# Optimization experiments

Measured on AMD Instinct MI355X. Metric: run time of the kernel, lower is better.

## Reference

```python
import jax, jax.numpy as jnp
import numpy as np

BIG = 1.0e9   # sentinel for masked distances / masked max
K_NBR = 64    # max_num_neighbors in radius()


def _fps(pos, n_sample):
    """Farthest point sampling on a single cloud pos [N, D] -> int32 [n_sample]."""
    n = pos.shape[0]

    def body(i, st):
        d, idxs = st
        last = pos[idxs[i - 1]]                              # [D]
        d = jnp.minimum(d, jnp.sum((pos - last) ** 2, axis=-1))
        return d, idxs.at[i].set(jnp.argmax(d).astype(jnp.int32))

    d0 = jnp.full((n,), BIG, pos.dtype)
    idxs0 = jnp.zeros((n_sample,), jnp.int32)
    _, idxs = jax.lax.fori_loop(1, n_sample, body, (d0, idxs0))
    return idxs


def _mlp2(h, w1, b1, w2, b2):
    # PyG MLP([a,b,c]) in eval mode (dropout off, batch-norm at default running
    # stats == identity): Linear -> ReLU -> Linear (plain last layer).
    return jax.nn.relu(h @ w1 + b1) @ w2 + b2


_gather = jax.vmap(lambda a, i: a[i])  # per-cloud fancy gather


def _sa(x, pos, ratio, r, w1, b1, w2, b2):
    """SAModule: FPS -> radius neighbors (<=K) -> PointConv (gather, MLP on
    [x_j, pos_j - pos_i], max-aggregate). Dense batched: x [B,N,C], pos [B,N,D]."""
    B, N, D = pos.shape
    M = int(round(N * ratio))
    idx = jax.vmap(lambda p: _fps(p, M))(pos)                 # [B, M]
    pos_q = _gather(pos, idx)                                 # [B, M, D]
    # pairwise squared distances query -> all points  [B, M, N]
    d2 = jnp.sum((pos_q[:, :, None, :] - pos[:, None, :, :]) ** 2, axis=-1)
    neg = jnp.where(d2 <= r * r, -d2, -BIG)
    vals, nbr = jax.lax.top_k(neg, K_NBR)                     # [B, M, K]
    valid = vals > -0.5 * BIG                                 # in-radius mask
    x_j = _gather(x, nbr)                                     # [B, M, K, C]
    rel = _gather(pos, nbr) - pos_q[:, :, None, :]            # [B, M, K, D]
    h = _mlp2(jnp.concatenate([x_j, rel], axis=-1), w1, b1, w2, b2)
    h = jnp.where(valid[..., None], h, -BIG)
    return jnp.max(h, axis=2), pos_q                          # max aggregation


def setup_inputs() -> dict:
    key = jax.random.key(0)
    ks = jax.random.split(key, 12)
    B, N, D, F = 8, 4096, 2, 5

    def lin(k, fi, fo):
        return (jax.random.normal(k, (fi, fo), jnp.float32) / np.sqrt(fi)).astype(jnp.float32)

    return {
        "x": jax.random.normal(ks[0], (B, N, F), jnp.float32),
        "pos": jax.random.uniform(ks[1], (B, N, D), jnp.float32),
        # sa1: MLP([5+2, 32, 64])
        "w1a": lin(ks[2], 7, 32),   "b1a": jnp.zeros((32,), jnp.float32),
        "w1b": lin(ks[3], 32, 64),  "b1b": jnp.zeros((64,), jnp.float32),
        # sa2: MLP([64+2, 64, 128])
        "w2a": lin(ks[4], 66, 64),  "b2a": jnp.zeros((64,), jnp.float32),
        "w2b": lin(ks[5], 64, 128), "b2b": jnp.zeros((128,), jnp.float32),
        # sa3 (global): MLP([128+2, 128, 256])
        "w3a": lin(ks[6], 130, 128), "b3a": jnp.zeros((128,), jnp.float32),
        "w3b": lin(ks[7], 128, 256), "b3b": jnp.zeros((256,), jnp.float32),
        # head: MLP([256, 256, 1024], norm=None)
        "w4a": lin(ks[8], 256, 256),  "b4a": jnp.zeros((256,), jnp.float32),
        "w4b": lin(ks[9], 256, 1024), "b4b": jnp.zeros((1024,), jnp.float32),
    }


def reference(x, pos, w1a, b1a, w1b, b1b, w2a, b2a, w2b, b2b,
              w3a, b3a, w3b, b3b, w4a, b4a, w4b, b4b):
    h1, p1 = _sa(x, pos, 0.5, 0.2, w1a, b1a, w1b, b1b)       # [B, N/2, 64]
    h2, p2 = _sa(h1, p1, 0.25, 0.4, w2a, b2a, w2b, b2b)      # [B, N/8, 128]
    g = _mlp2(jnp.concatenate([h2, p2], axis=-1), w3a, b3a, w3b, b3b)
    g = jnp.max(g, axis=1)                                    # global max pool [B, 256]
    return _mlp2(g, w4a, b4a, w4b, b4b)                       # [B, 1024]
```

## Files before the change

kernel.cpp:

```cpp
#include <hip/hip_runtime.h>


#define DPP_UMAX(u, ctrl)                                                      \
  do {                                                                         \
    unsigned _o = (unsigned)__builtin_amdgcn_update_dpp(0, (int)(u), (ctrl),   \
                                                        0xf, 0xf, true);       \
    (u) = ((u) > _o) ? (u) : _o;                                               \
  } while (0)

__device__ __forceinline__ uint4 kmax4(uint4 a, uint4 b) {
  unsigned long long ka = ((unsigned long long)a.y << 32) | a.x;
  unsigned long long kb = ((unsigned long long)b.y << 32) | b.x;
  bool c = kb > ka;
  uint4 r;
  r.x = c ? b.x : a.x; r.y = c ? b.y : a.y;
  r.z = c ? b.z : a.z; r.w = c ? b.w : a.w;
  return r;
}

template<int PPT, int T>
__device__ __forceinline__ void fps_stage(
    float (&xr)[PPT], float (&yr)[PPT], int Msel, int t,
    const float* srcx, const float* srcy,
    float* wlx, float* wly,
    uint4* slots ) {
  constexpr int NW = T / 64;
  constexpr int HP = PPT / 2;
  float lx = srcx[0], ly = srcy[0];
  if (t == 0) { wlx[0] = lx; wly[0] = ly; }
  float d[PPT];
#pragma unroll
  for (int k = 0; k < PPT; ++k) d[k] = 1e9f;

  for (int i = 1; i < Msel; ++i) {
#pragma unroll
    for (int k = 0; k < PPT; ++k) {
      float dx = xr[k] - lx, dy = yr[k] - ly;
      float dd = __fadd_rn(__fmul_rn(dx, dx), __fmul_rn(dy, dy));
      d[k] = fminf(d[k], dd);
    }
    float bvA = d[0]; int bkA = 0;
    float bvB = d[HP]; int bkB = HP;
#pragma unroll
    for (int k = 1; k < HP; ++k) {
      if (d[k] > bvA)      { bvA = d[k];      bkA = k; }
      if (d[HP + k] > bvB) { bvB = d[HP + k]; bkB = HP + k; }
    }
    float bv = bvA; int bk = bkA;
    if (bvB > bvA) { bv = bvB; bk = bkB; }
    const int cand = t * PPT + bk;
    const float cx = srcx[cand], cy = srcy[cand];
    const unsigned mybits = __float_as_uint(bv);
    unsigned u = mybits;
    DPP_UMAX(u, 0x111);
    DPP_UMAX(u, 0x112);
    DPP_UMAX(u, 0x114);
    DPP_UMAX(u, 0x118);
    DPP_UMAX(u, 0x142);
    DPP_UMAX(u, 0x143);
    const unsigned wvb = (unsigned)__builtin_amdgcn_readlane((int)u, 63);
    const unsigned long long tmask = __ballot(mybits == wvb);
    const int fl = (int)__builtin_ctzll(tmask);
    const int widx = __builtin_amdgcn_readlane(cand, fl);
    const unsigned wcx =
        (unsigned)__builtin_amdgcn_readlane((int)__float_as_uint(cx), fl);
    const unsigned wcy =
        (unsigned)__builtin_amdgcn_readlane((int)__float_as_uint(cy), fl);
    const int par = i & 1;
    if ((t & 63) == 0)
      slots[par * NW + (t >> 6)] = make_uint4(~(unsigned)widx, wvb, wcx, wcy);
    __syncthreads();
    const uint4* sl = &slots[par * NW];
    uint4 arr[NW];
#pragma unroll
    for (int j = 0; j < NW; ++j) arr[j] = sl[j];
#pragma unroll
    for (int s = NW / 2; s >= 1; s >>= 1)
#pragma unroll
      for (int j = 0; j < s; ++j) arr[j] = kmax4(arr[j], arr[j + s]);
    lx = __uint_as_float(arr[0].z);
    ly = __uint_as_float(arr[0].w);
    if (t == 0) { wlx[i] = lx; wly[i] = ly; }
  }
}

template<int N, int M1, int M2, int T>
__global__ __launch_bounds__(T, 1) void fps_fused_kernel(
    const float* __restrict__ pos,
    float* __restrict__ posq1,
    float* __restrict__ posq2) {
  constexpr int PPT  = N / T;
  constexpr int PPT2 = M1 / T;
  constexpr int NW   = T / 64;
  __shared__ float sx[N], sy[N];
  __shared__ float wlx[M1], wly[M1];
  __shared__ float wl2x[M2], wl2y[M2];
  __shared__ uint4 slots[2 * NW];
  const int b = blockIdx.x, t = threadIdx.x;
  float xr[PPT], yr[PPT];
  const float4* p4 = (const float4*)(pos + (size_t)b * N * 2 + (size_t)t * PPT * 2);
#pragma unroll
  for (int q = 0; q < PPT / 2; ++q) {
    float4 v = p4[q];
    xr[2 * q + 0] = v.x; yr[2 * q + 0] = v.y;
    xr[2 * q + 1] = v.z; yr[2 * q + 1] = v.w;
  }
#pragma unroll
  for (int k = 0; k < PPT; ++k) {
    int pt = t * PPT + k;
    sx[pt] = xr[k]; sy[pt] = yr[k];
  }
  __syncthreads();
  fps_stage<PPT, T>(xr, yr, M1, t, sx, sy, wlx, wly, slots);
  __syncthreads();
  for (int j = t; j < M1; j += T)
    ((float2*)posq1)[(size_t)b * M1 + j] = make_float2(wlx[j], wly[j]);
  float x2[PPT2], y2[PPT2];
#pragma unroll
  for (int k = 0; k < PPT2; ++k) { x2[k] = wlx[t * PPT2 + k]; y2[k] = wly[t * PPT2 + k]; }
  __syncthreads();
  fps_stage<PPT2, T>(x2, y2, M2, t, wlx, wly, wl2x, wl2y, slots);
  __syncthreads();
  for (int j = t; j < M2; j += T)
    ((float2*)posq2)[(size_t)b * M2 + j] = make_float2(wl2x[j], wl2y[j]);
}

template<int CPL>
__global__ __launch_bounds__(256) void nbr_kernel(
    const float* __restrict__ pts,
    const float* __restrict__ posq,
    int* __restrict__ nbr,
    int M, int NPTS, int total_q, float R2) {
  const int wid = blockIdx.x * 4 + (threadIdx.x >> 6);
  if (wid >= total_q) return;
  const int lane = threadIdx.x & 63;
  const int b = wid / M;
  const float qx = posq[(size_t)wid * 2 + 0], qy = posq[(size_t)wid * 2 + 1];
  const float* p = pts + (size_t)b * NPTS * 2;
  unsigned bits[CPL];
  int cnt = 0;
#pragma unroll
  for (int k = 0; k < CPL; ++k) {
    int pt = lane + (k << 6);
    float dx = p[pt * 2 + 0] - qx, dy = p[pt * 2 + 1] - qy;
    float dd = __fadd_rn(__fmul_rn(dx, dx), __fmul_rn(dy, dy));
    bool inr = (dd <= R2);
    bits[k] = inr ? __float_as_uint(dd) : 0xFFFFFFFFu;
    cnt += __popcll(__ballot(inr));
  }
  const unsigned long long below = (1ULL << lane) - 1ULL;
  if (cnt <= 64) {
    int base = 0;
#pragma unroll
    for (int k = 0; k < CPL; ++k) {
      bool s = (bits[k] != 0xFFFFFFFFu);
      unsigned long long m = __ballot(s);
      if (s) nbr[(size_t)wid * 64 + base + __popcll(m & below)] = lane + (k << 6);
      base += __popcll(m);
    }
    for (int j = base + lane; j < 64; j += 64) nbr[(size_t)wid * 64 + j] = -1;
  } else {
    unsigned lo = 0, hi = __float_as_uint(R2);
    while (lo < hi) {
      unsigned mid = lo + ((hi - lo) >> 1);
      int c = 0;
#pragma unroll
      for (int k = 0; k < CPL; ++k) c += __popcll(__ballot(bits[k] <= mid));
      if (c >= 64) hi = mid; else lo = mid + 1;
    }
    int cless = 0;
#pragma unroll
    for (int k = 0; k < CPL; ++k) cless += __popcll(__ballot(bits[k] < lo));
    const int need = 64 - cless;
    int base = 0, tiecnt = 0;
#pragma unroll
    for (int k = 0; k < CPL; ++k) {
      bool tie = (bits[k] == lo);
      unsigned long long tm = __ballot(tie);
      bool s = (bits[k] < lo) || (tie && (tiecnt + __popcll(tm & below)) < need);
      tiecnt += __popcll(tm);
      unsigned long long m = __ballot(s);
      if (s) nbr[(size_t)wid * 64 + base + __popcll(m & below)] = lane + (k << 6);
      base += __popcll(m);
    }
  }
}

template<int CIN, int H, int COUT, int QPB, int NPTS, int HS, int W1P>
__global__ __launch_bounds__(64 * QPB) void conv_kernel(
    const float* __restrict__ x,
    const float* __restrict__ pts,
    const float* __restrict__ posq,
    const int* __restrict__ nbr,
    const float* __restrict__ W1, const float* __restrict__ b1,
    const float* __restrict__ W2, const float* __restrict__ b2,
    float* __restrict__ out,
    int M) {
  constexpr int CI2 = CIN + 2;
  __shared__ float sW1t[H * W1P];
  __shared__ float sB1[H];
  __shared__ float sHH[QPB * 64 * HS];
  const int tid = threadIdx.x;
  for (int j = tid; j < CI2 * H; j += 64 * QPB) {
    int c = j / H, h = j - c * H;
    sW1t[h * W1P + c] = W1[j];
  }
  for (int j = tid; j < H; j += 64 * QPB) sB1[j] = b1[j];
  __syncthreads();
  const int wv = tid >> 6, lane = tid & 63;
  const int wid = blockIdx.x * QPB + wv;
  const int b = wid / M;
  const int idx = nbr[(size_t)wid * 64 + lane];
  const unsigned long long vm = __ballot(idx >= 0);
  const int ii = (idx < 0) ? 0 : idx;
  float in[CI2];
  {
    const float* xp = x + ((size_t)b * NPTS + ii) * CIN;
#pragma unroll
    for (int c = 0; c < CIN; ++c) in[c] = xp[c];
    float qx = posq[(size_t)wid * 2 + 0], qy = posq[(size_t)wid * 2 + 1];
    const float* pp = pts + ((size_t)b * NPTS + ii) * 2;
    in[CIN] = pp[0] - qx;
    in[CIN + 1] = pp[1] - qy;
  }
  float* hbase = &sHH[wv * 64 * HS];
#pragma unroll
  for (int h = 0; h < H; h += 4) {
    float vv[4];
#pragma unroll
    for (int j = 0; j < 4; ++j) {
      float a = sB1[h + j];
#pragma unroll
      for (int c = 0; c < CI2; ++c) a = fmaf(in[c], sW1t[(h + j) * W1P + c], a);
      vv[j] = fmaxf(a, 0.0f);
    }
    *(float4*)&hbase[lane * HS + h] = make_float4(vv[0], vv[1], vv[2], vv[3]);
  }
#pragma unroll
  for (int half = 0; half < COUT / 64; ++half) {
    const int o = half * 64 + lane;
    float w2r[H];
#pragma unroll
    for (int h = 0; h < H; ++h) w2r[h] = W2[h * COUT + o];
    const float b2o = b2[o];
    float m = -1e30f;
    for (int n = 0; n < 64; ++n) {
      const float4* hp = (const float4*)&hbase[n * HS];
      float a = b2o;
#pragma unroll
      for (int j = 0; j < H / 4; ++j) {
        float4 hv = hp[j];
        a = fmaf(hv.x, w2r[4 * j + 0], a);
        a = fmaf(hv.y, w2r[4 * j + 1], a);
        a = fmaf(hv.z, w2r[4 * j + 2], a);
        a = fmaf(hv.w, w2r[4 * j + 3], a);
      }
      a = ((vm >> n) & 1ULL) ? a : -1e9f;
      m = fmaxf(m, a);
    }
    out[(size_t)wid * COUT + o] = m;
  }
}

__global__ __launch_bounds__(256) void u_kernel(
    const float* __restrict__ h2,
    const float* __restrict__ posq2,
    const float* __restrict__ W3a, const float* __restrict__ b3a,
    float* __restrict__ u) {
  const int p = blockIdx.x * 2 + (threadIdx.x >> 7);
  const int h = threadIdx.x & 127;
  const float* hp = h2 + (size_t)p * 128;
  float a = b3a[h];
  for (int c = 0; c < 128; ++c) a = fmaf(hp[c], W3a[c * 128 + h], a);
  a = fmaf(posq2[(size_t)p * 2 + 0], W3a[128 * 128 + h], a);
  a = fmaf(posq2[(size_t)p * 2 + 1], W3a[129 * 128 + h], a);
  u[(size_t)p * 128 + h] = fmaxf(a, 0.0f);
}

__global__ __launch_bounds__(256) void g_kernel(
    const float* __restrict__ u,
    const float* __restrict__ W3b, const float* __restrict__ b3b,
    float* __restrict__ part) {
  __shared__ float su[64 * 128];
  const int bb = blockIdx.x;
  const float* up = u + (size_t)bb * 64 * 128;
  for (int j = threadIdx.x; j < 64 * 128; j += 256) su[j] = up[j];
  __syncthreads();
  const int o = threadIdx.x;
  float w[128];
#pragma unroll
  for (int h = 0; h < 128; ++h) w[h] = W3b[h * 256 + o];
  float m = -1e30f;
  for (int p = 0; p < 64; ++p) {
    float a = b3b[o];
    const float4* sp = (const float4*)&su[p * 128];
#pragma unroll
    for (int j = 0; j < 32; ++j) {
      float4 v = sp[j];
      a = fmaf(v.x, w[4 * j + 0], a);
      a = fmaf(v.y, w[4 * j + 1], a);
      a = fmaf(v.z, w[4 * j + 2], a);
      a = fmaf(v.w, w[4 * j + 3], a);
    }
    m = fmaxf(m, a);
  }
  part[(size_t)bb * 256 + o] = m;
}

__global__ __launch_bounds__(256) void head_kernel(
    const float* __restrict__ part,
    const float* __restrict__ W4a, const float* __restrict__ b4a,
    const float* __restrict__ W4b, const float* __restrict__ b4b,
    float* __restrict__ out) {
  __shared__ float g[256], h4[256];
  const int b = blockIdx.x, t = threadIdx.x;
  float m = part[(size_t)(b * 8 + 0) * 256 + t];
  for (int c = 1; c < 8; ++c) m = fmaxf(m, part[(size_t)(b * 8 + c) * 256 + t]);
  g[t] = m;
  __syncthreads();
  float a = b4a[t];
  for (int c = 0; c < 256; ++c) a = fmaf(g[c], W4a[c * 256 + t], a);
  h4[t] = fmaxf(a, 0.0f);
  __syncthreads();
  for (int jj = 0; jj < 4; ++jj) {
    int o = t + jj * 256;
    float a2 = b4b[o];
    for (int c = 0; c < 256; ++c) a2 = fmaf(h4[c], W4b[c * 1024 + o], a2);
    out[(size_t)b * 1024 + o] = a2;
  }
}

extern "C" void kernel_launch(void* const* d_in, const int* in_sizes, int n_in,
                              void* d_out, int out_size, void* d_ws, size_t ws_size,
                              hipStream_t stream) {
  (void)in_sizes; (void)n_in; (void)out_size; (void)ws_size;
  const float* x   = (const float*)d_in[0];
  const float* pos = (const float*)d_in[1];
  const float* w1a = (const float*)d_in[2];  const float* b1a = (const float*)d_in[3];
  const float* w1b = (const float*)d_in[4];  const float* b1b = (const float*)d_in[5];
  const float* w2a = (const float*)d_in[6];  const float* b2a = (const float*)d_in[7];
  const float* w2b = (const float*)d_in[8];  const float* b2b = (const float*)d_in[9];
  const float* w3a = (const float*)d_in[10]; const float* b3a = (const float*)d_in[11];
  const float* w3b = (const float*)d_in[12]; const float* b3b = (const float*)d_in[13];
  const float* w4a = (const float*)d_in[14]; const float* b4a = (const float*)d_in[15];
  const float* w4b = (const float*)d_in[16]; const float* b4b = (const float*)d_in[17];
  float* outp = (float*)d_out;

  char* ws = (char*)d_ws;
  size_t off = 0;
  float* posq1 = (float*)(ws + off); off += (size_t)8 * 2048 * 2 * 4;
  float* posq2 = (float*)(ws + off); off += (size_t)8 * 512 * 2 * 4;
  int*   nbr1  = (int*)  (ws + off); off += (size_t)16384 * 64 * 4;
  int*   nbr2  = (int*)  (ws + off); off += (size_t)4096 * 64 * 4;
  float* h1    = (float*)(ws + off); off += (size_t)16384 * 64 * 4;
  float* h2    = (float*)(ws + off); off += (size_t)4096 * 128 * 4;
  float* u3    = (float*)(ws + off); off += (size_t)4096 * 128 * 4;
  float* part  = (float*)(ws + off); off += (size_t)64 * 256 * 4;

  fps_fused_kernel<4096, 2048, 512, 512><<<dim3(8), dim3(512), 0, stream>>>(
      pos, posq1, posq2);
  nbr_kernel<64><<<dim3(4096), dim3(256), 0, stream>>>(pos, posq1, nbr1,
                                                       2048, 4096, 16384, 0.04f);
  conv_kernel<5, 32, 64, 4, 4096, 36, 8><<<dim3(4096), dim3(256), 0, stream>>>(
      x, pos, posq1, nbr1, w1a, b1a, w1b, b1b, h1, 2048);
  nbr_kernel<32><<<dim3(1024), dim3(256), 0, stream>>>(posq1, posq2, nbr2,
                                                       512, 2048, 4096, 0.16f);
  conv_kernel<64, 64, 128, 2, 2048, 68, 68><<<dim3(2048), dim3(128), 0, stream>>>(
      h1, posq1, posq2, nbr2, w2a, b2a, w2b, b2b, h2, 512);
  u_kernel<<<dim3(2048), dim3(256), 0, stream>>>(h2, posq2, w3a, b3a, u3);
  g_kernel<<<dim3(64), dim3(256), 0, stream>>>(u3, w3b, b3b, part);
  head_kernel<<<dim3(8), dim3(256), 0, stream>>>(part, w4a, b4a, w4b, b4b, outp);
}
```

Before: 2.387 ms.

## Carry FPS candidate coordinates in registers and halve the FPS block size

```diff
diff --git a/kernel.cpp b/kernel.cpp
--- a/kernel.cpp
+++ b/kernel.cpp
@@ -21,13 +21,12 @@
 template<int PPT, int T>
 __device__ __forceinline__ void fps_stage(
     float (&xr)[PPT], float (&yr)[PPT], int Msel, int t,
-    const float* srcx, const float* srcy,
+    float lx, float ly,
     float* wlx, float* wly,
     uint4* slots ) {
   constexpr int NW = T / 64;
   constexpr int HP = PPT / 2;
-  float lx = srcx[0], ly = srcy[0];
-  if (t == 0) { wlx[0] = lx; wly[0] = ly; }
+  const int wvid = t >> 6;
   float d[PPT];
 #pragma unroll
   for (int k = 0; k < PPT; ++k) d[k] = 1e9f;
@@ -39,17 +38,15 @@
       float dd = __fadd_rn(__fmul_rn(dx, dx), __fmul_rn(dy, dy));
       d[k] = fminf(d[k], dd);
     }
-    float bvA = d[0]; int bkA = 0;
-    float bvB = d[HP]; int bkB = HP;
+    float bvA = d[0],  bxA = xr[0],  byA = yr[0];
+    float bvB = d[HP], bxB = xr[HP], byB = yr[HP];
 #pragma unroll
     for (int k = 1; k < HP; ++k) {
-      if (d[k] > bvA)      { bvA = d[k];      bkA = k; }
-      if (d[HP + k] > bvB) { bvB = d[HP + k]; bkB = HP + k; }
-    }
-    float bv = bvA; int bk = bkA;
-    if (bvB > bvA) { bv = bvB; bk = bkB; }
-    const int cand = t * PPT + bk;
-    const float cx = srcx[cand], cy = srcy[cand];
+      if (d[k] > bvA)      { bvA = d[k];      bxA = xr[k];      byA = yr[k]; }
+      if (d[HP + k] > bvB) { bvB = d[HP + k]; bxB = xr[HP + k]; byB = yr[HP + k]; }
+    }
+    float bv = bvA, bx = bxA, by = byA;
+    if (bvB > bvA) { bv = bvB; bx = bxB; by = byB; }
     const unsigned mybits = __float_as_uint(bv);
     unsigned u = mybits;
     DPP_UMAX(u, 0x111);
@@ -61,14 +58,11 @@
     const unsigned wvb = (unsigned)__builtin_amdgcn_readlane((int)u, 63);
     const unsigned long long tmask = __ballot(mybits == wvb);
     const int fl = (int)__builtin_ctzll(tmask);
-    const int widx = __builtin_amdgcn_readlane(cand, fl);
-    const unsigned wcx =
-        (unsigned)__builtin_amdgcn_readlane((int)__float_as_uint(cx), fl);
-    const unsigned wcy =
-        (unsigned)__builtin_amdgcn_readlane((int)__float_as_uint(cy), fl);
     const int par = i & 1;
-    if ((t & 63) == 0)
-      slots[par * NW + (t >> 6)] = make_uint4(~(unsigned)widx, wvb, wcx, wcy);
+    if ((t & 63) == fl)
+      slots[par * NW + wvid] = make_uint4(~(unsigned)wvid, wvb,
+                                          __float_as_uint(bx),
+                                          __float_as_uint(by));
     __syncthreads();
     const uint4* sl = &slots[par * NW];
     uint4 arr[NW];
@@ -92,7 +86,6 @@
   constexpr int PPT  = N / T;
   constexpr int PPT2 = M1 / T;
   constexpr int NW   = T / 64;
-  __shared__ float sx[N], sy[N];
   __shared__ float wlx[M1], wly[M1];
   __shared__ float wl2x[M2], wl2y[M2];
   __shared__ uint4 slots[2 * NW];
@@ -105,21 +98,19 @@
     xr[2 * q + 0] = v.x; yr[2 * q + 0] = v.y;
     xr[2 * q + 1] = v.z; yr[2 * q + 1] = v.w;
   }
-#pragma unroll
-  for (int k = 0; k < PPT; ++k) {
-    int pt = t * PPT + k;
-    sx[pt] = xr[k]; sy[pt] = yr[k];
-  }
-  __syncthreads();
-  fps_stage<PPT, T>(xr, yr, M1, t, sx, sy, wlx, wly, slots);
+  if (t == 0) { wlx[0] = xr[0]; wly[0] = yr[0]; }
+  __syncthreads();
+  float lx = wlx[0], ly = wly[0];
+  fps_stage<PPT, T>(xr, yr, M1, t, lx, ly, wlx, wly, slots);
   __syncthreads();
   for (int j = t; j < M1; j += T)
     ((float2*)posq1)[(size_t)b * M1 + j] = make_float2(wlx[j], wly[j]);
   float x2[PPT2], y2[PPT2];
 #pragma unroll
   for (int k = 0; k < PPT2; ++k) { x2[k] = wlx[t * PPT2 + k]; y2[k] = wly[t * PPT2 + k]; }
-  __syncthreads();
-  fps_stage<PPT2, T>(x2, y2, M2, t, wlx, wly, wl2x, wl2y, slots);
+  float lx2 = wlx[0], ly2 = wly[0];
+  if (t == 0) { wl2x[0] = lx2; wl2y[0] = ly2; }
+  fps_stage<PPT2, T>(x2, y2, M2, t, lx2, ly2, wl2x, wl2y, slots);
   __syncthreads();
   for (int j = t; j < M2; j += T)
     ((float2*)posq2)[(size_t)b * M2 + j] = make_float2(wl2x[j], wl2y[j]);
@@ -357,7 +348,7 @@
   float* u3    = (float*)(ws + off); off += (size_t)4096 * 128 * 4;
   float* part  = (float*)(ws + off); off += (size_t)64 * 256 * 4;
 
-  fps_fused_kernel<4096, 2048, 512, 512><<<dim3(8), dim3(512), 0, stream>>>(
+  fps_fused_kernel<4096, 2048, 512, 256><<<dim3(8), dim3(256), 0, stream>>>(
       pos, posq1, posq2);
   nbr_kernel<64><<<dim3(4096), dim3(256), 0, stream>>>(pos, posq1, nbr1,
                                                        2048, 4096, 16384, 0.04f);
```

Result: faster. 2.159 ms (-9.5%).
